# Performance work log

Hardware: AMD Instinct MI355X
Metric: run time of the kernel (lower is better)

The kernel has to match this reference:

```python
import jax, jax.numpy as jnp
import numpy as np

EPSILON = 1e-13
LN_EPS = 1e-5
DIRECTIONS = 2
HID = 512


def setup_inputs() -> dict:
    key = jax.random.key(0)
    k1, k2, k3, k4 = jax.random.split(key, 4)
    B, N, D = 16, 1024, HID
    adj = jax.random.randint(k1, (B, N, N), 0, 3, dtype=jnp.int32)  # labels 0..2
    hid = jax.random.normal(k2, (B, N, D), dtype=jnp.float32)
    W = jax.random.normal(k3, (DIRECTIONS * D, D), dtype=jnp.float32) * (1.0 / np.sqrt(DIRECTIONS * D))
    b = jnp.zeros((D,), dtype=jnp.float32)
    gamma = jnp.ones((D,), dtype=jnp.float32)
    beta = jnp.zeros((D,), dtype=jnp.float32)
    return {"adj": adj, "hid": hid, "W": W, "b": b, "gamma": gamma, "beta": beta}


def _layer_norm(x, gamma, beta):
    mu = jnp.mean(x, axis=-1, keepdims=True)
    var = jnp.mean(jnp.square(x - mu), axis=-1, keepdims=True)
    return (x - mu) * jax.lax.rsqrt(var + LN_EPS) * gamma + beta


def reference(adj, hid, W, b, gamma, beta):
    residual = hid
    direct_list = []
    for j in range(DIRECTIONS):  # fixed small structural loop
        mask = (adj == (j + 1)).astype(hid.dtype)            # [B,N,N]
        weight = mask / (jnp.sum(mask, axis=-1, keepdims=True) + EPSILON)
        direct_list.append(jnp.einsum('bnm,bmd->bnd', weight, hid))
    out = jnp.concatenate(direct_list, axis=-1)              # [B,N,directions*D]
    out = out @ W + b                                        # [B,N,D]
    out = jax.nn.relu(out)
    out = out + residual
    return _layer_norm(out, gamma, beta)
```

## Files before the change

### kernel.cpp

```cpp
#include <hip/hip_runtime.h>

#define NB 16
#define NN 1024
#define ND 512

typedef __attribute__((ext_vector_type(8))) short short8;
typedef __attribute__((ext_vector_type(4))) float f32x4;

typedef const __attribute__((address_space(1))) void* gptr1;
typedef __attribute__((address_space(3))) void* lptr3;

#define VMCNT0() asm volatile("s_waitcnt vmcnt(0)" ::: "memory")
#define VMCNT8() asm volatile("s_waitcnt vmcnt(8)" ::: "memory")
#define LGKM0()  asm volatile("s_waitcnt lgkmcnt(0)" ::: "memory")
#define BAR()    __builtin_amdgcn_s_barrier()

union U8 { uint4 u; short8 s; };

static __device__ __forceinline__ unsigned f2bf(float f) {
  union { float f; unsigned u; } v; v.f = f;
  unsigned r = v.u + 0x7FFFu + ((v.u >> 16) & 1u);
  return r >> 16;
}
static __device__ __forceinline__ float bf2f(unsigned short h) {
  union { unsigned u; float f; } v; v.u = ((unsigned)h) << 16;
  return v.f;
}

__global__ void k_wt(const float* __restrict__ W, unsigned short* __restrict__ WT) {
  __shared__ float t[64][65];
  int r0 = blockIdx.x * 64;
  int c0 = blockIdx.y * 64;
  int tid = threadIdx.x;
#pragma unroll
  for (int i = 0; i < 4; ++i) {
    int f = i * 256 + tid;
    int r = f >> 4, cq = f & 15;
    float4 v = *(const float4*)(W + (size_t)(r0 + r) * ND + c0 + cq * 4);
    t[r][cq * 4 + 0] = v.x; t[r][cq * 4 + 1] = v.y;
    t[r][cq * 4 + 2] = v.z; t[r][cq * 4 + 3] = v.w;
  }
  __syncthreads();
#pragma unroll
  for (int i = 0; i < 8; ++i) {
    int f = i * 256 + tid;
    int oc = f >> 5;
    int on = (f & 31) * 2;
    unsigned lo = f2bf(t[on][oc]), hi = f2bf(t[on + 1][oc]);
    *(unsigned*)(WT + (size_t)(c0 + oc) * NN + r0 + on) = lo | (hi << 16);
  }
}

__global__ void k_pack(const int* __restrict__ adj, unsigned* __restrict__ packed,
                       float* __restrict__ invc) {
  int wid = threadIdx.x >> 6, lane = threadIdx.x & 63;
  int wrow0 = (blockIdx.x * 4 + wid) * 4;
#pragma unroll
  for (int r = 0; r < 4; ++r) {
    int row = wrow0 + r;
    const int* p = adj + (size_t)row * NN + lane * 16;
    unsigned u = 0;
#pragma unroll
    for (int i = 0; i < 4; ++i) {
      int4 v = *(const int4*)(p + i * 4);
      u |= ((unsigned)v.x << (8 * i)) | ((unsigned)v.y << (8 * i + 2))
         | ((unsigned)v.z << (8 * i + 4)) | ((unsigned)v.w << (8 * i + 6));
    }
    packed[(size_t)row * 64 + lane] = u;
    unsigned c1 = __popc(u & 0x55555555u);
    unsigned c2 = __popc(u & 0xAAAAAAAAu);
    unsigned pr = c1 | (c2 << 16);
#pragma unroll
    for (int o = 32; o; o >>= 1) pr += __shfl_xor(pr, o);
    if (lane == 0) {
      invc[row * 2 + 0] = 1.0f / ((float)(pr & 0xFFFFu) + 1e-13f);
      invc[row * 2 + 1] = 1.0f / ((float)(pr >> 16) + 1e-13f);
    }
  }
}

__global__ __launch_bounds__(256, 2) void k_pre(
    const float* __restrict__ hid, const unsigned short* __restrict__ WT,
    unsigned short* __restrict__ Pt1, unsigned short* __restrict__ Pt2) {
  __shared__ __align__(16) char smem[81920];

  int phys = blockIdx.x;
  int logical = (phys & 7) * 64 + (phys >> 3);
  int b = logical >> 5;
  int rem = logical & 31;
  int dt = rem >> 3, mt = rem & 7;
  int d0 = dt * 128, m0 = mt * 128;

  int tid = threadIdx.x, lane = tid & 63, wid = tid >> 6;
  int wr = wid >> 1, wc = wid & 1;
  int srow = lane >> 3;
  int ssl = (lane & 7) ^ srow;

  const float* hb = hid + (size_t)b * NN * ND;
  char* Bh = smem + 65536;

  f32x4 acc1[4][4], acc2[4][4];
  f32x4 zero = {0.f, 0.f, 0.f, 0.f};
#pragma unroll
  for (int i = 0; i < 4; ++i)
#pragma unroll
    for (int j = 0; j < 4; ++j) { acc1[i][j] = zero; acc2[i][j] = zero; }

  float4 fc[8], fn[8];
#pragma unroll
  for (int it = 0; it < 8; ++it) {
    int f = it * 256 + tid;
    fc[it] = *(const float4*)(hb + (size_t)(m0 + (f >> 4)) * ND + (f & 15) * 4);
  }
#pragma unroll
  for (int i = 0; i < 4; ++i) {
    int q = wid * 4 + i;
    int r = q * 8 + srow;
    __builtin_amdgcn_global_load_lds((gptr1)(WT + (size_t)(d0 + r) * NN + ssl * 8),
                                     (lptr3)(smem + q * 1024), 16, 0, 0);
    __builtin_amdgcn_global_load_lds((gptr1)(WT + (size_t)(d0 + r) * NN + 512 + ssl * 8),
                                     (lptr3)(smem + 16384 + q * 1024), 16, 0, 0);
  }

#pragma unroll 1
  for (int kt = 0; kt < 8; ++kt) {
    int k0 = kt * 64;
#pragma unroll
    for (int it = 0; it < 8; ++it) {
      int f = it * 256 + tid;
      int row = f >> 4, colq = f & 15;
      float4 v = fc[it];
      unsigned lo = f2bf(v.x) | (f2bf(v.y) << 16);
      unsigned hi = f2bf(v.z) | (f2bf(v.w) << 16);
      int addr = row * 128 + (((colq >> 1) ^ (row & 7)) * 16) + (colq & 1) * 8;
      *(uint2*)(Bh + addr) = make_uint2(lo, hi);
    }
    if (kt < 7) {
#pragma unroll
      for (int it = 0; it < 8; ++it) {
        int f = it * 256 + tid;
        fn[it] = *(const float4*)(hb + (size_t)(m0 + (f >> 4)) * ND + k0 + 64 + (f & 15) * 4);
      }
    }
    if (kt == 7) { VMCNT0(); } else { VMCNT8(); }
    LGKM0();
    BAR();
    if (kt < 7) {
      char* ab = smem + (((kt + 1) & 1) << 15);
#pragma unroll
      for (int i = 0; i < 4; ++i) {
        int q = wid * 4 + i;
        int r = q * 8 + srow;
        __builtin_amdgcn_global_load_lds((gptr1)(WT + (size_t)(d0 + r) * NN + k0 + 64 + ssl * 8),
                                         (lptr3)(ab + q * 1024), 16, 0, 0);
        __builtin_amdgcn_global_load_lds((gptr1)(WT + (size_t)(d0 + r) * NN + 512 + k0 + 64 + ssl * 8),
                                         (lptr3)(ab + 16384 + q * 1024), 16, 0, 0);
      }
    }
    const char* ac = smem + ((kt & 1) << 15);
#pragma unroll
    for (int ks = 0; ks < 2; ++ks) {
      short8 a1[4], a2[4], bf[4];
#pragma unroll
      for (int mi = 0; mi < 4; ++mi) {
        int row = wr * 64 + mi * 16 + (lane & 15);
        int slot = (ks * 4 + (lane >> 4)) ^ (row & 7);
        a1[mi] = *(const short8*)(ac + row * 128 + slot * 16);
        a2[mi] = *(const short8*)(ac + 16384 + row * 128 + slot * 16);
      }
#pragma unroll
      for (int nj = 0; nj < 4; ++nj) {
        int col = wc * 64 + nj * 16 + (lane & 15);
        int slot = (ks * 4 + (lane >> 4)) ^ (col & 7);
        bf[nj] = *(const short8*)(Bh + col * 128 + slot * 16);
      }
#pragma unroll
      for (int mi = 0; mi < 4; ++mi)
#pragma unroll
        for (int nj = 0; nj < 4; ++nj) {
          acc1[mi][nj] = __builtin_amdgcn_mfma_f32_16x16x32_bf16(a1[mi], bf[nj], acc1[mi][nj], 0, 0, 0);
          acc2[mi][nj] = __builtin_amdgcn_mfma_f32_16x16x32_bf16(a2[mi], bf[nj], acc2[mi][nj], 0, 0, 0);
        }
    }
    BAR();
    if (kt < 7) {
#pragma unroll
      for (int it = 0; it < 8; ++it) fc[it] = fn[it];
    }
    __builtin_amdgcn_sched_barrier(0);
  }
  unsigned short* P1b = Pt1 + (size_t)b * ND * NN;
  unsigned short* P2b = Pt2 + (size_t)b * ND * NN;
#pragma unroll
  for (int mi = 0; mi < 4; ++mi) {
#pragma unroll
    for (int rr = 0; rr < 4; ++rr) {
      int rowd = d0 + wr * 64 + mi * 16 + (lane >> 4) * 4 + rr;
#pragma unroll
      for (int nj = 0; nj < 4; ++nj) {
        int colm = m0 + wc * 64 + nj * 16 + (lane & 15);
        P1b[(size_t)rowd * NN + colm] = (unsigned short)f2bf(acc1[mi][nj][rr]);
        P2b[(size_t)rowd * NN + colm] = (unsigned short)f2bf(acc2[mi][nj][rr]);
      }
    }
  }
}

__global__ __launch_bounds__(256, 2) void k_main(
    const unsigned* __restrict__ packed, const unsigned short* __restrict__ Pt1,
    const unsigned short* __restrict__ Pt2, const float* __restrict__ invc,
    const float* __restrict__ bias, const float* __restrict__ hid,
    unsigned short* __restrict__ preS) {
  __shared__ __align__(16) char smem[65536];

  int phys = blockIdx.x;
  int logical = (phys & 7) * 64 + (phys >> 3);
  int b = logical >> 5;
  int rem = logical & 31;
  int mt = rem >> 2, nt = rem & 3;
  int n0 = mt * 128, d0 = nt * 128;

  int tid = threadIdx.x, lane = tid & 63, wid = tid >> 6;
  int wr = wid >> 1, wc = wid & 1;
  int l15 = lane & 15, lq = lane >> 4;
  unsigned sh = (lq & 1) << 4;
  int srow = lane >> 3;
  int ssl = (lane & 7) ^ srow;

  const unsigned* cp[4];
#pragma unroll
  for (int mi = 0; mi < 4; ++mi)
    cp[mi] = packed + ((size_t)b * NN + n0 + wr * 64 + mi * 16 + l15) * 64 + (lq >> 1);

  const unsigned short* pb1 = Pt1 + ((size_t)b * ND + d0) * NN;
  const unsigned short* pb2 = Pt2 + ((size_t)b * ND + d0) * NN;

  f32x4 acc1[4][4], acc2[4][4];
  f32x4 zero = {0.f, 0.f, 0.f, 0.f};
#pragma unroll
  for (int i = 0; i < 4; ++i)
#pragma unroll
    for (int j = 0; j < 4; ++j) { acc1[i][j] = zero; acc2[i][j] = zero; }

  unsigned cr[4][2], ncr[4][2];
#pragma unroll
  for (int mi = 0; mi < 4; ++mi) { cr[mi][0] = cp[mi][0]; cr[mi][1] = cp[mi][2]; }

#pragma unroll
  for (int i = 0; i < 4; ++i) {
    int q = wid * 4 + i;
    size_t ro = (size_t)(q * 8 + srow) * NN + ssl * 8;
    __builtin_amdgcn_global_load_lds((gptr1)(pb1 + ro), (lptr3)(smem + q * 1024), 16, 0, 0);
    __builtin_amdgcn_global_load_lds((gptr1)(pb2 + ro), (lptr3)(smem + 16384 + q * 1024), 16, 0, 0);
  }
#pragma unroll
  for (int i = 0; i < 4; ++i) {
    int q = wid * 4 + i;
    size_t ro = (size_t)(q * 8 + srow) * NN + 64 + ssl * 8;
    __builtin_amdgcn_global_load_lds((gptr1)(pb1 + ro), (lptr3)(smem + 32768 + q * 1024), 16, 0, 0);
    __builtin_amdgcn_global_load_lds((gptr1)(pb2 + ro), (lptr3)(smem + 49152 + q * 1024), 16, 0, 0);
  }

#pragma unroll 1
  for (int kt = 0; kt < 16; ++kt) {
    if (kt == 15) { VMCNT0(); } else { VMCNT8(); }
    BAR();
    if (kt < 15) {
#pragma unroll
      for (int mi = 0; mi < 4; ++mi) { ncr[mi][0] = cp[mi][4]; ncr[mi][1] = cp[mi][6]; }
    }
    const char* bb = smem + ((kt & 1) << 15);
#pragma unroll
    for (int ks = 0; ks < 2; ++ks) {
      U8 a[4];
#pragma unroll
      for (int mi = 0; mi < 4; ++mi) {
        unsigned h = cr[mi][ks] >> sh;
#pragma unroll
        for (int j = 0; j < 4; ++j) {
          unsigned t = (h >> (4 * j)) & 5u;
          a[mi].u[j] = ((t | (t << 14)) & 0x00010001u) * 0x3F80u;
        }
      }
      short8 bfr[4];
#pragma unroll
      for (int nj = 0; nj < 4; ++nj) {
        int col = wc * 64 + nj * 16 + l15;
        int slot = (ks * 4 + lq) ^ (col & 7);
        bfr[nj] = *(const short8*)(bb + col * 128 + slot * 16);
      }
#pragma unroll
      for (int nj = 0; nj < 4; ++nj)
#pragma unroll
        for (int mi = 0; mi < 4; ++mi)
          acc1[mi][nj] = __builtin_amdgcn_mfma_f32_16x16x32_bf16(a[mi].s, bfr[nj], acc1[mi][nj], 0, 0, 0);
#pragma unroll
      for (int mi = 0; mi < 4; ++mi) {
        unsigned h = cr[mi][ks] >> sh;
#pragma unroll
        for (int j = 0; j < 4; ++j) {
          unsigned t = (h >> (4 * j + 1)) & 5u;
          a[mi].u[j] = ((t | (t << 14)) & 0x00010001u) * 0x3F80u;
        }
      }
#pragma unroll
      for (int nj = 0; nj < 4; ++nj) {
        int col = wc * 64 + nj * 16 + l15;
        int slot = (ks * 4 + lq) ^ (col & 7);
        bfr[nj] = *(const short8*)(bb + 16384 + col * 128 + slot * 16);
      }
#pragma unroll
      for (int nj = 0; nj < 4; ++nj)
#pragma unroll
        for (int mi = 0; mi < 4; ++mi)
          acc2[mi][nj] = __builtin_amdgcn_mfma_f32_16x16x32_bf16(a[mi].s, bfr[nj], acc2[mi][nj], 0, 0, 0);
    }
    BAR();
    if (kt < 14) {
      char* sb = (char*)smem + ((kt & 1) << 15);
      int k0n = kt * 64 + 128;
#pragma unroll
      for (int i = 0; i < 4; ++i) {
        int q = wid * 4 + i;
        size_t ro = (size_t)(q * 8 + srow) * NN + k0n + ssl * 8;
        __builtin_amdgcn_global_load_lds((gptr1)(pb1 + ro), (lptr3)(sb + q * 1024), 16, 0, 0);
        __builtin_amdgcn_global_load_lds((gptr1)(pb2 + ro), (lptr3)(sb + 16384 + q * 1024), 16, 0, 0);
      }
    }
    if (kt < 15) {
#pragma unroll
      for (int mi = 0; mi < 4; ++mi) {
        cr[mi][0] = ncr[mi][0]; cr[mi][1] = ncr[mi][1];
        cp[mi] += 4;
      }
    }
    __builtin_amdgcn_sched_barrier(0);
  }

#pragma unroll
  for (int mi = 0; mi < 4; ++mi) {
#pragma unroll
    for (int rr = 0; rr < 4; ++rr) {
      int n = n0 + wr * 64 + mi * 16 + lq * 4 + rr;
      float i1 = invc[((size_t)b * NN + n) * 2 + 0];
      float i2 = invc[((size_t)b * NN + n) * 2 + 1];
      const float* hrow = hid + ((size_t)b * NN + n) * ND;
      unsigned short* prow = preS + ((size_t)b * NN + n) * ND;
#pragma unroll
      for (int nj = 0; nj < 4; ++nj) {
        int d = d0 + wc * 64 + nj * 16 + l15;
        float v = acc1[mi][nj][rr] * i1 + acc2[mi][nj][rr] * i2 + bias[d];
        v = fmaxf(v, 0.f);
        v += hrow[d];
        prow[d] = (unsigned short)f2bf(v);
      }
    }
  }
}

__global__ void k_ln(const unsigned short* __restrict__ preS, float* __restrict__ out,
                     const float* __restrict__ gamma, const float* __restrict__ beta) {
  int row = blockIdx.x * 4 + (threadIdx.x >> 6);
  int lane = threadIdx.x & 63;
  short8 raw = *(const short8*)(preS + (size_t)row * ND + lane * 8);
  float x[8];
#pragma unroll
  for (int i = 0; i < 8; ++i) x[i] = bf2f((unsigned short)raw[i]);
  float s = 0.f;
#pragma unroll
  for (int i = 0; i < 8; ++i) s += x[i];
#pragma unroll
  for (int o = 32; o; o >>= 1) s += __shfl_xor(s, o);
  float mu = s * (1.0f / 512.0f);
  float v = 0.f;
#pragma unroll
  for (int i = 0; i < 8; ++i) { float d = x[i] - mu; v += d * d; }
#pragma unroll
  for (int o = 32; o; o >>= 1) v += __shfl_xor(v, o);
  float rs = rsqrtf(v * (1.0f / 512.0f) + 1e-5f);
  float4 g0 = *(const float4*)(gamma + lane * 8);
  float4 g1 = *(const float4*)(gamma + lane * 8 + 4);
  float4 b0 = *(const float4*)(beta + lane * 8);
  float4 b1 = *(const float4*)(beta + lane * 8 + 4);
  float4 y0, y1;
  y0.x = (x[0] - mu) * rs * g0.x + b0.x; y0.y = (x[1] - mu) * rs * g0.y + b0.y;
  y0.z = (x[2] - mu) * rs * g0.z + b0.z; y0.w = (x[3] - mu) * rs * g0.w + b0.w;
  y1.x = (x[4] - mu) * rs * g1.x + b1.x; y1.y = (x[5] - mu) * rs * g1.y + b1.y;
  y1.z = (x[6] - mu) * rs * g1.z + b1.z; y1.w = (x[7] - mu) * rs * g1.w + b1.w;
  float* p = out + (size_t)row * ND + lane * 8;
  *(float4*)p = y0;
  *(float4*)(p + 4) = y1;
}

extern "C" void kernel_launch(void* const* d_in, const int* in_sizes, int n_in,
                              void* d_out, int out_size, void* d_ws, size_t ws_size,
                              hipStream_t stream) {
  (void)in_sizes; (void)n_in; (void)out_size; (void)ws_size;
  const int*   adj   = (const int*)d_in[0];
  const float* hid   = (const float*)d_in[1];
  const float* W     = (const float*)d_in[2];
  const float* bias  = (const float*)d_in[3];
  const float* gamma = (const float*)d_in[4];
  const float* beta  = (const float*)d_in[5];
  float* out = (float*)d_out;

  char* ws = (char*)d_ws;
  unsigned short* WT     = (unsigned short*)ws;
  unsigned short* Pt1    = (unsigned short*)(ws + 1048576);
  unsigned short* Pt2    = (unsigned short*)(ws + 17825792);
  unsigned*       packed = (unsigned*)(ws + 34603008);
  float*          invc   = (float*)(ws + 38797312);
  unsigned short* preS   = (unsigned short*)(ws + 38928384);

  k_wt  <<<dim3(16, 8), 256, 0, stream>>>(W, WT);
  k_pack<<<1024, 256, 0, stream>>>(adj, packed, invc);
  k_pre <<<512, 256, 0, stream>>>(hid, WT, Pt1, Pt2);
  k_main<<<512, 256, 0, stream>>>(packed, Pt1, Pt2, invc, bias, hid, preS);
  k_ln  <<<4096, 256, 0, stream>>>(preS, out, gamma, beta);
}
```

Baseline: 120.9 us.

## Decode adjacency masks once into LDS and use single-barrier K=32 pipeline

Each thread now decodes one packed adjacency word per K-step into bf16 mask tiles stored in LDS. Previously every wave decoded its own mask fragments in registers, so the same bits were expanded redundantly across waves. The K loop moves from 64-wide steps with two barriers to 32-wide steps with one barrier. Prefetch is issued at the top of each iteration and the loop waits on vmcnt(0) at the end. This cuts redundant ALU decode and register pressure, but doubles the iteration count and adds LDS writes and reads for the A operand. The full vmcnt drain each step may also expose global load latency.

```diff
diff --git a/kernel.cpp b/kernel.cpp
--- a/kernel.cpp
+++ b/kernel.cpp
@@ -15,8 +15,6 @@
 #define LGKM0()  asm volatile("s_waitcnt lgkmcnt(0)" ::: "memory")
 #define BAR()    __builtin_amdgcn_s_barrier()
 
-union U8 { uint4 u; short8 s; };
-
 static __device__ __forceinline__ unsigned f2bf(float f) {
   union { float f; unsigned u; } v; v.f = f;
   unsigned r = v.u + 0x7FFFu + ((v.u >> 16) & 1u);
@@ -25,6 +23,10 @@
 static __device__ __forceinline__ float bf2f(unsigned short h) {
   union { unsigned u; float f; } v; v.u = ((unsigned)h) << 16;
   return v.f;
+}
+static __device__ __forceinline__ unsigned mk2(unsigned w, int sh) {
+  unsigned t = (w >> sh) & 5u;
+  return ((t | (t << 14)) & 0x00010001u) * 0x3F80u;
 }
 
 __global__ void k_wt(const float* __restrict__ W, unsigned short* __restrict__ WT) {
@@ -212,6 +214,8 @@
     const float* __restrict__ bias, const float* __restrict__ hid,
     unsigned short* __restrict__ preS) {
   __shared__ __align__(16) char smem[65536];
+  char* smA = smem;
+  char* smB = smem + 32768;
 
   int phys = blockIdx.x;
   int logical = (phys & 7) * 64 + (phys >> 3);
@@ -223,18 +227,15 @@
   int tid = threadIdx.x, lane = tid & 63, wid = tid >> 6;
   int wr = wid >> 1, wc = wid & 1;
   int l15 = lane & 15, lq = lane >> 4;
-  unsigned sh = (lq & 1) << 4;
-  int srow = lane >> 3;
-  int ssl = (lane & 7) ^ srow;
-
-  const unsigned* cp[4];
-#pragma unroll
-  for (int mi = 0; mi < 4; ++mi)
-    cp[mi] = packed + ((size_t)b * NN + n0 + wr * 64 + mi * 16 + l15) * 64 + (lq >> 1);
-
+  int rowown = tid >> 1, h = tid & 1;
+
+  const unsigned* cpp = packed + ((size_t)b * NN + n0 + rowown) * 64 + h;
   const unsigned short* pb1 = Pt1 + ((size_t)b * ND + d0) * NN;
   const unsigned short* pb2 = Pt2 + ((size_t)b * ND + d0) * NN;
 
+  int srow = lane >> 2;
+  int scol = (lane & 3) * 8;
+
   f32x4 acc1[4][4], acc2[4][4];
   f32x4 zero = {0.f, 0.f, 0.f, 0.f};
 #pragma unroll
@@ -242,98 +243,76 @@
 #pragma unroll
     for (int j = 0; j < 4; ++j) { acc1[i][j] = zero; acc2[i][j] = zero; }
 
-  unsigned cr[4][2], ncr[4][2];
-#pragma unroll
-  for (int mi = 0; mi < 4; ++mi) { cr[mi][0] = cp[mi][0]; cr[mi][1] = cp[mi][2]; }
-
-#pragma unroll
-  for (int i = 0; i < 4; ++i) {
-    int q = wid * 4 + i;
-    size_t ro = (size_t)(q * 8 + srow) * NN + ssl * 8;
-    __builtin_amdgcn_global_load_lds((gptr1)(pb1 + ro), (lptr3)(smem + q * 1024), 16, 0, 0);
-    __builtin_amdgcn_global_load_lds((gptr1)(pb2 + ro), (lptr3)(smem + 16384 + q * 1024), 16, 0, 0);
-  }
-#pragma unroll
-  for (int i = 0; i < 4; ++i) {
-    int q = wid * 4 + i;
-    size_t ro = (size_t)(q * 8 + srow) * NN + 64 + ssl * 8;
-    __builtin_amdgcn_global_load_lds((gptr1)(pb1 + ro), (lptr3)(smem + 32768 + q * 1024), 16, 0, 0);
-    __builtin_amdgcn_global_load_lds((gptr1)(pb2 + ro), (lptr3)(smem + 49152 + q * 1024), 16, 0, 0);
-  }
+  unsigned c_cur = cpp[0];
+#pragma unroll
+  for (int i = 0; i < 2; ++i) {
+    int q = wid * 2 + i;
+    size_t ro = (size_t)(q * 16 + srow) * NN + scol;
+    __builtin_amdgcn_global_load_lds((gptr1)(pb1 + ro), (lptr3)(smB + q * 1024), 16, 0, 0);
+    __builtin_amdgcn_global_load_lds((gptr1)(pb2 + ro), (lptr3)(smB + 8192 + q * 1024), 16, 0, 0);
+  }
+  {
+    char* wp = smA + rowown * 64 + h * 32;
+    uint4 x0, x1, y0, y1;
+    x0.x = mk2(c_cur, 0);  x0.y = mk2(c_cur, 4);  x0.z = mk2(c_cur, 8);  x0.w = mk2(c_cur, 12);
+    x1.x = mk2(c_cur, 16); x1.y = mk2(c_cur, 20); x1.z = mk2(c_cur, 24); x1.w = mk2(c_cur, 28);
+    y0.x = mk2(c_cur, 1);  y0.y = mk2(c_cur, 5);  y0.z = mk2(c_cur, 9);  y0.w = mk2(c_cur, 13);
+    y1.x = mk2(c_cur, 17); y1.y = mk2(c_cur, 21); y1.z = mk2(c_cur, 25); y1.w = mk2(c_cur, 29);
+    *(uint4*)wp = x0; *(uint4*)(wp + 16) = x1;
+    *(uint4*)(wp + 8192) = y0; *(uint4*)(wp + 8192 + 16) = y1;
+  }
+  unsigned c_nxt = cpp[2];
+  LGKM0(); VMCNT0(); BAR();
 
 #pragma unroll 1
-  for (int kt = 0; kt < 16; ++kt) {
-    if (kt == 15) { VMCNT0(); } else { VMCNT8(); }
-    BAR();
-    if (kt < 15) {
-#pragma unroll
-      for (int mi = 0; mi < 4; ++mi) { ncr[mi][0] = cp[mi][4]; ncr[mi][1] = cp[mi][6]; }
-    }
-    const char* bb = smem + ((kt & 1) << 15);
-#pragma unroll
-    for (int ks = 0; ks < 2; ++ks) {
-      U8 a[4];
-#pragma unroll
-      for (int mi = 0; mi < 4; ++mi) {
-        unsigned h = cr[mi][ks] >> sh;
-#pragma unroll
-        for (int j = 0; j < 4; ++j) {
-          unsigned t = (h >> (4 * j)) & 5u;
-          a[mi].u[j] = ((t | (t << 14)) & 0x00010001u) * 0x3F80u;
-        }
-      }
-      short8 bfr[4];
-#pragma unroll
-      for (int nj = 0; nj < 4; ++nj) {
-        int col = wc * 64 + nj * 16 + l15;
-        int slot = (ks * 4 + lq) ^ (col & 7);
-        bfr[nj] = *(const short8*)(bb + col * 128 + slot * 16);
-      }
-#pragma unroll
-      for (int nj = 0; nj < 4; ++nj)
-#pragma unroll
-        for (int mi = 0; mi < 4; ++mi)
-          acc1[mi][nj] = __builtin_amdgcn_mfma_f32_16x16x32_bf16(a[mi].s, bfr[nj], acc1[mi][nj], 0, 0, 0);
-#pragma unroll
-      for (int mi = 0; mi < 4; ++mi) {
-        unsigned h = cr[mi][ks] >> sh;
-#pragma unroll
-        for (int j = 0; j < 4; ++j) {
-          unsigned t = (h >> (4 * j + 1)) & 5u;
-          a[mi].u[j] = ((t | (t << 14)) & 0x00010001u) * 0x3F80u;
-        }
-      }
-#pragma unroll
-      for (int nj = 0; nj < 4; ++nj) {
-        int col = wc * 64 + nj * 16 + l15;
-        int slot = (ks * 4 + lq) ^ (col & 7);
-        bfr[nj] = *(const short8*)(bb + 16384 + col * 128 + slot * 16);
-      }
-#pragma unroll
-      for (int nj = 0; nj < 4; ++nj)
-#pragma unroll
-        for (int mi = 0; mi < 4; ++mi)
-          acc2[mi][nj] = __builtin_amdgcn_mfma_f32_16x16x32_bf16(a[mi].s, bfr[nj], acc2[mi][nj], 0, 0, 0);
-    }
-    BAR();
-    if (kt < 14) {
-      char* sb = (char*)smem + ((kt & 1) << 15);
-      int k0n = kt * 64 + 128;
-#pragma unroll
-      for (int i = 0; i < 4; ++i) {
-        int q = wid * 4 + i;
-        size_t ro = (size_t)(q * 8 + srow) * NN + k0n + ssl * 8;
-        __builtin_amdgcn_global_load_lds((gptr1)(pb1 + ro), (lptr3)(sb + q * 1024), 16, 0, 0);
-        __builtin_amdgcn_global_load_lds((gptr1)(pb2 + ro), (lptr3)(sb + 16384 + q * 1024), 16, 0, 0);
-      }
-    }
-    if (kt < 15) {
-#pragma unroll
-      for (int mi = 0; mi < 4; ++mi) {
-        cr[mi][0] = ncr[mi][0]; cr[mi][1] = ncr[mi][1];
-        cp[mi] += 4;
-      }
-    }
+  for (int kt = 0; kt < 32; ++kt) {
+    int cb = (kt & 1) << 14;
+    int nb = cb ^ 16384;
+    if (kt < 31) {
+      int k0n = (kt + 1) * 32;
+#pragma unroll
+      for (int i = 0; i < 2; ++i) {
+        int q = wid * 2 + i;
+        size_t ro = (size_t)(q * 16 + srow) * NN + k0n + scol;
+        __builtin_amdgcn_global_load_lds((gptr1)(pb1 + ro), (lptr3)(smB + nb + q * 1024), 16, 0, 0);
+        __builtin_amdgcn_global_load_lds((gptr1)(pb2 + ro), (lptr3)(smB + nb + 8192 + q * 1024), 16, 0, 0);
+      }
+    }
+    short8 a1[4], a2[4], b1f[4], b2f[4];
+#pragma unroll
+    for (int mi = 0; mi < 4; ++mi) {
+      int r = wr * 64 + mi * 16 + l15;
+      a1[mi] = *(const short8*)(smA + cb + r * 64 + lq * 16);
+      a2[mi] = *(const short8*)(smA + cb + 8192 + r * 64 + lq * 16);
+    }
+#pragma unroll
+    for (int nj = 0; nj < 4; ++nj) {
+      int c = wc * 64 + nj * 16 + l15;
+      b1f[nj] = *(const short8*)(smB + cb + c * 64 + lq * 16);
+      b2f[nj] = *(const short8*)(smB + cb + 8192 + c * 64 + lq * 16);
+    }
+    if (kt < 31) {
+      char* wp = smA + nb + rowown * 64 + h * 32;
+      uint4 x0, x1, y0, y1;
+      x0.x = mk2(c_nxt, 0);  x0.y = mk2(c_nxt, 4);  x0.z = mk2(c_nxt, 8);  x0.w = mk2(c_nxt, 12);
+      x1.x = mk2(c_nxt, 16); x1.y = mk2(c_nxt, 20); x1.z = mk2(c_nxt, 24); x1.w = mk2(c_nxt, 28);
+      y0.x = mk2(c_nxt, 1);  y0.y = mk2(c_nxt, 5);  y0.z = mk2(c_nxt, 9);  y0.w = mk2(c_nxt, 13);
+      y1.x = mk2(c_nxt, 17); y1.y = mk2(c_nxt, 21); y1.z = mk2(c_nxt, 25); y1.w = mk2(c_nxt, 29);
+      *(uint4*)wp = x0; *(uint4*)(wp + 16) = x1;
+      *(uint4*)(wp + 8192) = y0; *(uint4*)(wp + 8192 + 16) = y1;
+      if (kt < 30) c_nxt = cpp[(kt + 2) * 2];
+    }
+#pragma unroll
+    for (int nj = 0; nj < 4; ++nj)
+#pragma unroll
+      for (int mi = 0; mi < 4; ++mi)
+        acc1[mi][nj] = __builtin_amdgcn_mfma_f32_16x16x32_bf16(a1[mi], b1f[nj], acc1[mi][nj], 0, 0, 0);
+#pragma unroll
+    for (int nj = 0; nj < 4; ++nj)
+#pragma unroll
+      for (int mi = 0; mi < 4; ++mi)
+        acc2[mi][nj] = __builtin_amdgcn_mfma_f32_16x16x32_bf16(a2[mi], b2f[nj], acc2[mi][nj], 0, 0, 0);
+    LGKM0(); VMCNT0(); BAR();
     __builtin_amdgcn_sched_barrier(0);
   }
 
```

New measurement: 111.6 us. 1.08x faster.

## Concatenate direction weights and restructure pre/main GEMMs to single-accumulator tiles

Applied to the files above, without the earlier changes.

Stores both direction weight transposes in one concatenated [1024x512] matrix. The projection kernel now runs 1024 blocks, each computing one 128x128 output tile with a single accumulator set, and uses less LDS. The aggregation kernel walks a 32-step K loop covering both directions in turn, with a smaller double-buffered LDS tile, and switches accumulators halfway. The goal is lower register and LDS pressure so more blocks fit per CU and latency hides better; s_setprio is added around the MFMA sections. The cost is more, smaller tiles and a longer serial K loop in the main kernel, with preS reusing the WT workspace region.

```diff
diff --git a/kernel.cpp b/kernel.cpp
--- a/kernel.cpp
+++ b/kernel.cpp
@@ -27,8 +27,9 @@
   return v.f;
 }
 
-__global__ void k_wt(const float* __restrict__ W, unsigned short* __restrict__ WT) {
+__global__ void k_wtcat(const float* __restrict__ W, unsigned short* __restrict__ WTcat) {
   __shared__ float t[64][65];
+  int dir = blockIdx.z;
   int r0 = blockIdx.x * 64;
   int c0 = blockIdx.y * 64;
   int tid = threadIdx.x;
@@ -36,7 +37,7 @@
   for (int i = 0; i < 4; ++i) {
     int f = i * 256 + tid;
     int r = f >> 4, cq = f & 15;
-    float4 v = *(const float4*)(W + (size_t)(r0 + r) * ND + c0 + cq * 4);
+    float4 v = *(const float4*)(W + (size_t)(dir * 512 + r0 + r) * ND + c0 + cq * 4);
     t[r][cq * 4 + 0] = v.x; t[r][cq * 4 + 1] = v.y;
     t[r][cq * 4 + 2] = v.z; t[r][cq * 4 + 3] = v.w;
   }
@@ -47,7 +48,7 @@
     int oc = f >> 5;
     int on = (f & 31) * 2;
     unsigned lo = f2bf(t[on][oc]), hi = f2bf(t[on + 1][oc]);
-    *(unsigned*)(WT + (size_t)(c0 + oc) * NN + r0 + on) = lo | (hi << 16);
+    *(unsigned*)(WTcat + (size_t)(dir * 512 + c0 + oc) * ND + r0 + on) = lo | (hi << 16);
   }
 }
 
@@ -80,261 +81,238 @@
 }
 
 __global__ __launch_bounds__(256, 2) void k_pre(
-    const float* __restrict__ hid, const unsigned short* __restrict__ WT,
-    unsigned short* __restrict__ Pt1, unsigned short* __restrict__ Pt2) {
-  __shared__ __align__(16) char smem[81920];
+    const float* __restrict__ hid, const unsigned short* __restrict__ WTcat,
+    unsigned short* __restrict__ Ptcat) {
+  __shared__ __align__(16) char smem[49152];
+  char* Bh = smem + 32768;
+
+  int phys = blockIdx.x;
+  int logical = (phys & 7) * 128 + (phys >> 3);
+  int b = logical >> 6;
+  int rem = logical & 63;
+  int rt = rem >> 3, mt = rem & 7;
+  int r0 = rt * 128, m0 = mt * 128;
+
+  int tid = threadIdx.x, lane = tid & 63, wid = tid >> 6;
+  int wr = wid >> 1, wc = wid & 1;
+  int l15 = lane & 15, lq = lane >> 4;
+  int srow = lane >> 3;
+  int ssl = (lane & 7) ^ srow;
+
+  const float* hb = hid + (size_t)b * NN * ND;
+
+  f32x4 acc[4][4];
+  f32x4 zero = {0.f, 0.f, 0.f, 0.f};
+#pragma unroll
+  for (int i = 0; i < 4; ++i)
+#pragma unroll
+    for (int j = 0; j < 4; ++j) acc[i][j] = zero;
+
+  float4 fc[8], fn[8];
+#pragma unroll
+  for (int it = 0; it < 8; ++it) {
+    int f = it * 256 + tid;
+    fc[it] = *(const float4*)(hb + (size_t)(m0 + (f >> 4)) * ND + (f & 15) * 4);
+  }
+#pragma unroll
+  for (int i = 0; i < 4; ++i) {
+    int q = wid * 4 + i;
+    int r = q * 8 + srow;
+    __builtin_amdgcn_global_load_lds((gptr1)(WTcat + (size_t)(r0 + r) * ND + ssl * 8),
+                                     (lptr3)(smem + q * 1024), 16, 0, 0);
+  }
+
+#pragma unroll 1
+  for (int kt = 0; kt < 8; ++kt) {
+    int k0 = kt * 64;
+#pragma unroll
+    for (int it = 0; it < 8; ++it) {
+      int f = it * 256 + tid;
+      int row = f >> 4, c4 = f & 15;
+      float4 v = fc[it];
+      unsigned lo = f2bf(v.x) | (f2bf(v.y) << 16);
+      unsigned hi = f2bf(v.z) | (f2bf(v.w) << 16);
+      int addr = row * 128 + (((c4 >> 1) ^ (row & 7)) * 16) + (c4 & 1) * 8;
+      *(uint2*)(Bh + addr) = make_uint2(lo, hi);
+    }
+    if (kt < 7) {
+#pragma unroll
+      for (int it = 0; it < 8; ++it) {
+        int f = it * 256 + tid;
+        fn[it] = *(const float4*)(hb + (size_t)(m0 + (f >> 4)) * ND + k0 + 64 + (f & 15) * 4);
+      }
+      VMCNT8();
+    } else {
+      VMCNT0();
+    }
+    LGKM0();
+    BAR();
+    if (kt < 7) {
+      char* ab = smem + (((kt + 1) & 1) << 14);
+#pragma unroll
+      for (int i = 0; i < 4; ++i) {
+        int q = wid * 4 + i;
+        int r = q * 8 + srow;
+        __builtin_amdgcn_global_load_lds((gptr1)(WTcat + (size_t)(r0 + r) * ND + k0 + 64 + ssl * 8),
+                                         (lptr3)(ab + q * 1024), 16, 0, 0);
+      }
+    }
+    const char* ac = smem + ((kt & 1) << 14);
+    __builtin_amdgcn_s_setprio(1);
+#pragma unroll
+    for (int ks = 0; ks < 2; ++ks) {
+      short8 a[4], bf[4];
+#pragma unroll
+      for (int mi = 0; mi < 4; ++mi) {
+        int row = wr * 64 + mi * 16 + l15;
+        int slot = (ks * 4 + lq) ^ (l15 & 7);
+        a[mi] = *(const short8*)(ac + row * 128 + slot * 16);
+      }
+#pragma unroll
+      for (int nj = 0; nj < 4; ++nj) {
+        int col = wc * 64 + nj * 16 + l15;
+        int slot = (ks * 4 + lq) ^ (l15 & 7);
+        bf[nj] = *(const short8*)(Bh + col * 128 + slot * 16);
+      }
+#pragma unroll
+      for (int mi = 0; mi < 4; ++mi)
+#pragma unroll
+        for (int nj = 0; nj < 4; ++nj)
+          acc[mi][nj] = __builtin_amdgcn_mfma_f32_16x16x32_bf16(a[mi], bf[nj], acc[mi][nj], 0, 0, 0);
+    }
+    __builtin_amdgcn_s_setprio(0);
+    BAR();
+    if (kt < 7) {
+#pragma unroll
+      for (int it = 0; it < 8; ++it) fc[it] = fn[it];
+    }
+    __builtin_amdgcn_sched_barrier(0);
+  }
+  unsigned short* Pb = Ptcat + (size_t)b * NN * NN;
+#pragma unroll
+  for (int mi = 0; mi < 4; ++mi) {
+#pragma unroll
+    for (int rr = 0; rr < 4; ++rr) {
+      int r = r0 + wr * 64 + mi * 16 + lq * 4 + rr;
+#pragma unroll
+      for (int nj = 0; nj < 4; ++nj) {
+        int m = m0 + wc * 64 + nj * 16 + l15;
+        Pb[(size_t)r * NN + m] = (unsigned short)f2bf(acc[mi][nj][rr]);
+      }
+    }
+  }
+}
+
+__global__ __launch_bounds__(256, 2) void k_main(
+    const unsigned* __restrict__ packed, const unsigned short* __restrict__ Ptcat,
+    const float* __restrict__ invc, const float* __restrict__ bias,
+    const float* __restrict__ hid, unsigned short* __restrict__ preS) {
+  __shared__ __align__(16) char smB[32768];
 
   int phys = blockIdx.x;
   int logical = (phys & 7) * 64 + (phys >> 3);
   int b = logical >> 5;
   int rem = logical & 31;
-  int dt = rem >> 3, mt = rem & 7;
-  int d0 = dt * 128, m0 = mt * 128;
-
-  int tid = threadIdx.x, lane = tid & 63, wid = tid >> 6;
-  int wr = wid >> 1, wc = wid & 1;
-  int srow = lane >> 3;
-  int ssl = (lane & 7) ^ srow;
-
-  const float* hb = hid + (size_t)b * NN * ND;
-  char* Bh = smem + 65536;
-
-  f32x4 acc1[4][4], acc2[4][4];
-  f32x4 zero = {0.f, 0.f, 0.f, 0.f};
-#pragma unroll
-  for (int i = 0; i < 4; ++i)
-#pragma unroll
-    for (int j = 0; j < 4; ++j) { acc1[i][j] = zero; acc2[i][j] = zero; }
-
-  float4 fc[8], fn[8];
-#pragma unroll
-  for (int it = 0; it < 8; ++it) {
-    int f = it * 256 + tid;
-    fc[it] = *(const float4*)(hb + (size_t)(m0 + (f >> 4)) * ND + (f & 15) * 4);
-  }
-#pragma unroll
-  for (int i = 0; i < 4; ++i) {
-    int q = wid * 4 + i;
-    int r = q * 8 + srow;
-    __builtin_amdgcn_global_load_lds((gptr1)(WT + (size_t)(d0 + r) * NN + ssl * 8),
-                                     (lptr3)(smem + q * 1024), 16, 0, 0);
-    __builtin_amdgcn_global_load_lds((gptr1)(WT + (size_t)(d0 + r) * NN + 512 + ssl * 8),
-                                     (lptr3)(smem + 16384 + q * 1024), 16, 0, 0);
-  }
-
-#pragma unroll 1
-  for (int kt = 0; kt < 8; ++kt) {
-    int k0 = kt * 64;
-#pragma unroll
-    for (int it = 0; it < 8; ++it) {
-      int f = it * 256 + tid;
-      int row = f >> 4, colq = f & 15;
-      float4 v = fc[it];
-      unsigned lo = f2bf(v.x) | (f2bf(v.y) << 16);
-      unsigned hi = f2bf(v.z) | (f2bf(v.w) << 16);
-      int addr = row * 128 + (((colq >> 1) ^ (row & 7)) * 16) + (colq & 1) * 8;
-      *(uint2*)(Bh + addr) = make_uint2(lo, hi);
-    }
-    if (kt < 7) {
-#pragma unroll
-      for (int it = 0; it < 8; ++it) {
-        int f = it * 256 + tid;
-        fn[it] = *(const float4*)(hb + (size_t)(m0 + (f >> 4)) * ND + k0 + 64 + (f & 15) * 4);
-      }
-    }
-    if (kt == 7) { VMCNT0(); } else { VMCNT8(); }
-    LGKM0();
-    BAR();
-    if (kt < 7) {
-      char* ab = smem + (((kt + 1) & 1) << 15);
-#pragma unroll
-      for (int i = 0; i < 4; ++i) {
-        int q = wid * 4 + i;
-        int r = q * 8 + srow;
-        __builtin_amdgcn_global_load_lds((gptr1)(WT + (size_t)(d0 + r) * NN + k0 + 64 + ssl * 8),
-                                         (lptr3)(ab + q * 1024), 16, 0, 0);
-        __builtin_amdgcn_global_load_lds((gptr1)(WT + (size_t)(d0 + r) * NN + 512 + k0 + 64 + ssl * 8),
-                                         (lptr3)(ab + 16384 + q * 1024), 16, 0, 0);
-      }
-    }
-    const char* ac = smem + ((kt & 1) << 15);
-#pragma unroll
-    for (int ks = 0; ks < 2; ++ks) {
-      short8 a1[4], a2[4], bf[4];
-#pragma unroll
-      for (int mi = 0; mi < 4; ++mi) {
-        int row = wr * 64 + mi * 16 + (lane & 15);
-        int slot = (ks * 4 + (lane >> 4)) ^ (row & 7);
-        a1[mi] = *(const short8*)(ac + row * 128 + slot * 16);
-        a2[mi] = *(const short8*)(ac + 16384 + row * 128 + slot * 16);
-      }
-#pragma unroll
-      for (int nj = 0; nj < 4; ++nj) {
-        int col = wc * 64 + nj * 16 + (lane & 15);
-        int slot = (ks * 4 + (lane >> 4)) ^ (col & 7);
-        bf[nj] = *(const short8*)(Bh + col * 128 + slot * 16);
-      }
-#pragma unroll
-      for (int mi = 0; mi < 4; ++mi)
-#pragma unroll
-        for (int nj = 0; nj < 4; ++nj) {
-          acc1[mi][nj] = __builtin_amdgcn_mfma_f32_16x16x32_bf16(a1[mi], bf[nj], acc1[mi][nj], 0, 0, 0);
-          acc2[mi][nj] = __builtin_amdgcn_mfma_f32_16x16x32_bf16(a2[mi], bf[nj], acc2[mi][nj], 0, 0, 0);
-        }
-    }
-    BAR();
-    if (kt < 7) {
-#pragma unroll
-      for (int it = 0; it < 8; ++it) fc[it] = fn[it];
-    }
-    __builtin_amdgcn_sched_barrier(0);
-  }
-  unsigned short* P1b = Pt1 + (size_t)b * ND * NN;
-  unsigned short* P2b = Pt2 + (size_t)b * ND * NN;
-#pragma unroll
-  for (int mi = 0; mi < 4; ++mi) {
-#pragma unroll
-    for (int rr = 0; rr < 4; ++rr) {
-      int rowd = d0 + wr * 64 + mi * 16 + (lane >> 4) * 4 + rr;
-#pragma unroll
-      for (int nj = 0; nj < 4; ++nj) {
-        int colm = m0 + wc * 64 + nj * 16 + (lane & 15);
-        P1b[(size_t)rowd * NN + colm] = (unsigned short)f2bf(acc1[mi][nj][rr]);
-        P2b[(size_t)rowd * NN + colm] = (unsigned short)f2bf(acc2[mi][nj][rr]);
-      }
-    }
-  }
-}
-
-__global__ __launch_bounds__(256, 2) void k_main(
-    const unsigned* __restrict__ packed, const unsigned short* __restrict__ Pt1,
-    const unsigned short* __restrict__ Pt2, const float* __restrict__ invc,
-    const float* __restrict__ bias, const float* __restrict__ hid,
-    unsigned short* __restrict__ preS) {
-  __shared__ __align__(16) char smem[65536];
-
-  int phys = blockIdx.x;
-  int logical = (phys & 7) * 64 + (phys >> 3);
-  int b = logical >> 5;
-  int rem = logical & 31;
-  int mt = rem >> 2, nt = rem & 3;
-  int n0 = mt * 128, d0 = nt * 128;
+  int mt = rem >> 2, dt = rem & 3;
+  int n0 = mt * 128, d0 = dt * 128;
 
   int tid = threadIdx.x, lane = tid & 63, wid = tid >> 6;
   int wr = wid >> 1, wc = wid & 1;
   int l15 = lane & 15, lq = lane >> 4;
-  unsigned sh = (lq & 1) << 4;
   int srow = lane >> 3;
   int ssl = (lane & 7) ^ srow;
+  size_t bN = (size_t)b * NN;
 
   const unsigned* cp[4];
 #pragma unroll
   for (int mi = 0; mi < 4; ++mi)
-    cp[mi] = packed + ((size_t)b * NN + n0 + wr * 64 + mi * 16 + l15) * 64 + (lq >> 1);
-
-  const unsigned short* pb1 = Pt1 + ((size_t)b * ND + d0) * NN;
-  const unsigned short* pb2 = Pt2 + ((size_t)b * ND + d0) * NN;
-
-  f32x4 acc1[4][4], acc2[4][4];
+    cp[mi] = packed + (bN + n0 + wr * 64 + mi * 16 + l15) * 64 + (lq >> 1);
+
+  const unsigned short* Ptb = Ptcat + bN * NN;
+
+  const char* base0 = smB + (wc * 64 + l15) * 128 + ((lq ^ (l15 & 7)) * 16);
+  const char* base1 = smB + (wc * 64 + l15) * 128 + (((4 + lq) ^ (l15 & 7)) * 16);
+
+  f32x4 accA[4][4], accB[4][4];
   f32x4 zero = {0.f, 0.f, 0.f, 0.f};
 #pragma unroll
   for (int i = 0; i < 4; ++i)
 #pragma unroll
-    for (int j = 0; j < 4; ++j) { acc1[i][j] = zero; acc2[i][j] = zero; }
-
-  unsigned cr[4][2], ncr[4][2];
-#pragma unroll
-  for (int mi = 0; mi < 4; ++mi) { cr[mi][0] = cp[mi][0]; cr[mi][1] = cp[mi][2]; }
+    for (int j = 0; j < 4; ++j) { accA[i][j] = zero; accB[i][j] = zero; }
 
 #pragma unroll
   for (int i = 0; i < 4; ++i) {
     int q = wid * 4 + i;
-    size_t ro = (size_t)(q * 8 + srow) * NN + ssl * 8;
-    __builtin_amdgcn_global_load_lds((gptr1)(pb1 + ro), (lptr3)(smem + q * 1024), 16, 0, 0);
-    __builtin_amdgcn_global_load_lds((gptr1)(pb2 + ro), (lptr3)(smem + 16384 + q * 1024), 16, 0, 0);
-  }
-#pragma unroll
-  for (int i = 0; i < 4; ++i) {
-    int q = wid * 4 + i;
-    size_t ro = (size_t)(q * 8 + srow) * NN + 64 + ssl * 8;
-    __builtin_amdgcn_global_load_lds((gptr1)(pb1 + ro), (lptr3)(smem + 32768 + q * 1024), 16, 0, 0);
-    __builtin_amdgcn_global_load_lds((gptr1)(pb2 + ro), (lptr3)(smem + 49152 + q * 1024), 16, 0, 0);
-  }
-
+    __builtin_amdgcn_global_load_lds((gptr1)(Ptb + (size_t)(d0 + q * 8 + srow) * NN + ssl * 8),
+                                     (lptr3)(smB + q * 1024), 16, 0, 0);
+  }
+  unsigned cc[8], cn[8];
+#pragma unroll
+  for (int mi = 0; mi < 4; ++mi) { cc[mi * 2] = cp[mi][0]; cc[mi * 2 + 1] = cp[mi][2]; }
+
+  unsigned tgl = 0;
 #pragma unroll 1
-  for (int kt = 0; kt < 16; ++kt) {
-    if (kt == 15) { VMCNT0(); } else { VMCNT8(); }
+  for (int kt = 0; kt < 32; ++kt) {
+    VMCNT8();
     BAR();
-    if (kt < 15) {
-#pragma unroll
-      for (int mi = 0; mi < 4; ++mi) { ncr[mi][0] = cp[mi][4]; ncr[mi][1] = cp[mi][6]; }
-    }
-    const char* bb = smem + ((kt & 1) << 15);
-#pragma unroll
-    for (int ks = 0; ks < 2; ++ks) {
-      U8 a[4];
-#pragma unroll
-      for (int mi = 0; mi < 4; ++mi) {
-        unsigned h = cr[mi][ks] >> sh;
-#pragma unroll
-        for (int j = 0; j < 4; ++j) {
-          unsigned t = (h >> (4 * j)) & 5u;
-          a[mi].u[j] = ((t | (t << 14)) & 0x00010001u) * 0x3F80u;
-        }
-      }
-      short8 bfr[4];
-#pragma unroll
-      for (int nj = 0; nj < 4; ++nj) {
-        int col = wc * 64 + nj * 16 + l15;
-        int slot = (ks * 4 + lq) ^ (col & 7);
-        bfr[nj] = *(const short8*)(bb + col * 128 + slot * 16);
-      }
-#pragma unroll
-      for (int nj = 0; nj < 4; ++nj)
-#pragma unroll
-        for (int mi = 0; mi < 4; ++mi)
-          acc1[mi][nj] = __builtin_amdgcn_mfma_f32_16x16x32_bf16(a[mi].s, bfr[nj], acc1[mi][nj], 0, 0, 0);
-#pragma unroll
-      for (int mi = 0; mi < 4; ++mi) {
-        unsigned h = cr[mi][ks] >> sh;
-#pragma unroll
-        for (int j = 0; j < 4; ++j) {
-          unsigned t = (h >> (4 * j + 1)) & 5u;
-          a[mi].u[j] = ((t | (t << 14)) & 0x00010001u) * 0x3F80u;
-        }
-      }
-#pragma unroll
-      for (int nj = 0; nj < 4; ++nj) {
-        int col = wc * 64 + nj * 16 + l15;
-        int slot = (ks * 4 + lq) ^ (col & 7);
-        bfr[nj] = *(const short8*)(bb + 16384 + col * 128 + slot * 16);
-      }
-#pragma unroll
-      for (int nj = 0; nj < 4; ++nj)
-#pragma unroll
-        for (int mi = 0; mi < 4; ++mi)
-          acc2[mi][nj] = __builtin_amdgcn_mfma_f32_16x16x32_bf16(a[mi].s, bfr[nj], acc2[mi][nj], 0, 0, 0);
-    }
-    BAR();
-    if (kt < 14) {
-      char* sb = (char*)smem + ((kt & 1) << 15);
-      int k0n = kt * 64 + 128;
+    if (kt < 31) {
+      int t = kt + 1;
+      int dirn = t >> 4;
+      int k0n = (t & 15) * 64;
 #pragma unroll
       for (int i = 0; i < 4; ++i) {
         int q = wid * 4 + i;
-        size_t ro = (size_t)(q * 8 + srow) * NN + k0n + ssl * 8;
-        __builtin_amdgcn_global_load_lds((gptr1)(pb1 + ro), (lptr3)(sb + q * 1024), 16, 0, 0);
-        __builtin_amdgcn_global_load_lds((gptr1)(pb2 + ro), (lptr3)(sb + 16384 + q * 1024), 16, 0, 0);
-      }
-    }
-    if (kt < 15) {
+        __builtin_amdgcn_global_load_lds(
+            (gptr1)(Ptb + (size_t)(dirn * 512 + d0 + q * 8 + srow) * NN + k0n + ssl * 8),
+            (lptr3)(smB + (tgl ^ 16384) + q * 1024), 16, 0, 0);
+      }
+      int cw = (t & 15) * 4;
 #pragma unroll
       for (int mi = 0; mi < 4; ++mi) {
-        cr[mi][0] = ncr[mi][0]; cr[mi][1] = ncr[mi][1];
-        cp[mi] += 4;
-      }
-    }
-    __builtin_amdgcn_sched_barrier(0);
+        cn[mi * 2]     = cp[mi][cw];
+        cn[mi * 2 + 1] = cp[mi][cw + 2];
+      }
+    }
+    int dir = kt >> 4;
+    unsigned shb = (unsigned)((lq & 1) * 16 + dir);
+#pragma unroll
+    for (int ks = 0; ks < 2; ++ks) {
+      short8 bf[4];
+      const char* bs = (ks == 0) ? base0 : base1;
+#pragma unroll
+      for (int nj = 0; nj < 4; ++nj)
+        bf[nj] = *(const short8*)(bs + tgl + nj * 2048);
+      U8 a[4];
+#pragma unroll
+      for (int mi = 0; mi < 4; ++mi) {
+        unsigned cd = cc[mi * 2 + ks] >> shb;
+#pragma unroll
+        for (int j = 0; j < 4; ++j) {
+          unsigned t5 = (cd >> (4 * j)) & 5u;
+          a[mi].u[j] = ((t5 | (t5 << 14)) & 0x00010001u) * 0x3F80u;
+        }
+      }
+      __builtin_amdgcn_s_setprio(1);
+      if (kt < 16) {
+#pragma unroll
+        for (int nj = 0; nj < 4; ++nj)
+#pragma unroll
+          for (int mi = 0; mi < 4; ++mi)
+            accA[mi][nj] = __builtin_amdgcn_mfma_f32_16x16x32_bf16(a[mi].s, bf[nj], accA[mi][nj], 0, 0, 0);
+      } else {
+#pragma unroll
+        for (int nj = 0; nj < 4; ++nj)
+#pragma unroll
+          for (int mi = 0; mi < 4; ++mi)
+            accB[mi][nj] = __builtin_amdgcn_mfma_f32_16x16x32_bf16(a[mi].s, bf[nj], accB[mi][nj], 0, 0, 0);
+      }
+      __builtin_amdgcn_s_setprio(0);
+    }
+    if (kt < 31) {
+#pragma unroll
+      for (int i = 0; i < 8; ++i) cc[i] = cn[i];
+    }
+    tgl ^= 16384;
   }
 
 #pragma unroll
@@ -342,14 +320,14 @@
 #pragma unroll
     for (int rr = 0; rr < 4; ++rr) {
       int n = n0 + wr * 64 + mi * 16 + lq * 4 + rr;
-      float i1 = invc[((size_t)b * NN + n) * 2 + 0];
-      float i2 = invc[((size_t)b * NN + n) * 2 + 1];
-      const float* hrow = hid + ((size_t)b * NN + n) * ND;
-      unsigned short* prow = preS + ((size_t)b * NN + n) * ND;
+      float i1 = invc[(bN + n) * 2 + 0];
+      float i2 = invc[(bN + n) * 2 + 1];
+      const float* hrow = hid + (bN + n) * ND;
+      unsigned short* prow = preS + (bN + n) * ND;
 #pragma unroll
       for (int nj = 0; nj < 4; ++nj) {
         int d = d0 + wc * 64 + nj * 16 + l15;
-        float v = acc1[mi][nj][rr] * i1 + acc2[mi][nj][rr] * i2 + bias[d];
+        float v = accA[mi][nj][rr] * i1 + accB[mi][nj][rr] * i2 + bias[d];
         v = fmaxf(v, 0.f);
         v += hrow[d];
         prow[d] = (unsigned short)f2bf(v);
@@ -405,16 +383,15 @@
   float* out = (float*)d_out;
 
   char* ws = (char*)d_ws;
-  unsigned short* WT     = (unsigned short*)ws;
-  unsigned short* Pt1    = (unsigned short*)(ws + 1048576);
-  unsigned short* Pt2    = (unsigned short*)(ws + 17825792);
-  unsigned*       packed = (unsigned*)(ws + 34603008);
-  float*          invc   = (float*)(ws + 38797312);
-  unsigned short* preS   = (unsigned short*)(ws + 38928384);
-
-  k_wt  <<<dim3(16, 8), 256, 0, stream>>>(W, WT);
-  k_pack<<<1024, 256, 0, stream>>>(adj, packed, invc);
-  k_pre <<<512, 256, 0, stream>>>(hid, WT, Pt1, Pt2);
-  k_main<<<512, 256, 0, stream>>>(packed, Pt1, Pt2, invc, bias, hid, preS);
-  k_ln  <<<4096, 256, 0, stream>>>(preS, out, gamma, beta);
-}
+  unsigned short* WTcat  = (unsigned short*)ws;
+  unsigned short* preS   = (unsigned short*)ws;
+  unsigned short* Ptcat  = (unsigned short*)(ws + 16777216);
+  unsigned*       packed = (unsigned*)(ws + 50331648);
+  float*          invc   = (float*)(ws + 54525952);
+
+  k_wtcat<<<dim3(8, 8, 2), 256, 0, stream>>>(W, WTcat);
+  k_pack <<<1024, 256, 0, stream>>>(adj, packed, invc);
+  k_pre  <<<1024, 256, 0, stream>>>(hid, WTcat, Ptcat);
+  k_main <<<512, 256, 0, stream>>>(packed, Ptcat, invc, bias, hid, preS);
+  k_ln   <<<4096, 256, 0, stream>>>(preS, out, gamma, beta);
+}
```

Result: slower. 193.3 us (+59.9%).
